# Optimization experiments

Hardware: AMD Instinct MI355X
Metric: run time of the kernel (lower is better)

## Reference

```python
import jax, jax.numpy as jnp
import numpy as np

N_NODES = 50000
N_EDGES = 1600000
HID = 64
CUT_D = 4.0   # cutoff_distance
CUT_ON = 3.8  # cutoff_onset


def setup_inputs() -> dict:
    key = jax.random.key(0)
    ks = jax.random.split(key, 12)
    x = jax.random.normal(ks[0], (N_NODES, HID), jnp.float32)
    x0 = jax.random.normal(ks[1], (N_NODES, HID), jnp.float32)
    y = jax.random.normal(ks[2], (N_EDGES, HID), jnp.float32)
    # bond lengths in [0, 5) to exercise the smooth cutoff region around 3.8-4.0
    bondlength = jax.random.uniform(ks[3], (N_EDGES,), jnp.float32) * 5.0
    src = jax.random.randint(ks[4], (N_EDGES,), 0, N_NODES, jnp.int32)
    dst = jax.random.randint(ks[5], (N_EDGES,), 0, N_NODES, jnp.int32)
    s = 1.0 / np.sqrt(HID)
    Wsg = jax.random.normal(ks[6], (HID, 1), jnp.float32) * s
    Wdg = jax.random.normal(ks[7], (HID, 1), jnp.float32) * s
    Weg = jax.random.normal(ks[8], (HID, 1), jnp.float32) * s
    Wsp = jax.random.normal(ks[9], (HID, 4), jnp.float32) * s
    Wdp = jax.random.normal(ks[10], (HID, 4), jnp.float32) * s
    bsg = jnp.zeros((1,), jnp.float32)
    bdg = jnp.zeros((1,), jnp.float32)
    beg = jnp.zeros((1,), jnp.float32)
    bsp = jnp.zeros((4,), jnp.float32)  # = log([1,1,1,1])
    return dict(x=x, x0=x0, y=y, bondlength=bondlength, src=src, dst=dst,
                Wsg=Wsg, bsg=bsg, Wdg=Wdg, bdg=bdg, Weg=Weg, beg=beg,
                Wsp=Wsp, bsp=bsp, Wdp=Wdp)


def _cutoff(r):
    D = 0.5 * (CUT_D - CUT_ON)  # 0.1
    R = CUT_D - D               # 3.9
    c = jnp.where(r < R - D, jnp.ones_like(r),
                  0.5 - 0.5 * jnp.sin(jnp.pi * (r - R) / (2 * D)))
    return jnp.where(r > R + D, jnp.zeros_like(r), c)


def reference(x, x0, y, bondlength, src, dst,
              Wsg, bsg, Wdg, bdg, Weg, beg, Wsp, bsp, Wdp):
    # BondOrderConv: per-edge gated sigmoid (u_add_v of node gates + edge gate)
    e_src = x @ Wsg + bsg          # [N,1]
    e_dst = x @ Wdg + bdg          # [N,1]
    m = e_src[src] + e_dst[dst] + (y @ Weg + beg)  # [E,1]
    bond_order = jax.nn.sigmoid(m)[:, 0]           # [E]

    # BondOrderInteraction: pairwise params via u_add_v, then pair potential
    p_src = x0 @ Wsp + bsp         # [N,4]
    p_dst = x0 @ Wdp               # [N,4] (no bias)
    params = jnp.exp(p_src[src] + p_dst[dst])      # [E,4]
    f_repulse = params[:, 0] * jnp.exp(-params[:, 1] * bondlength)
    f_attract = params[:, 2] * jnp.exp(-params[:, 3] * bondlength)
    V_pair = _cutoff(bondlength) * (f_repulse - bond_order * f_attract)  # [E]

    # copy_e / sum: scatter-add edge energies onto destination nodes
    atomwise_energy = jax.ops.segment_sum(V_pair, dst, num_segments=N_NODES)
    # AvgPooling readout (energy_units == 'eV/atom', single graph)
    energy = jnp.mean(atomwise_energy)
    return energy, atomwise_energy
```

## Files before the change

kernel.cpp:

```cpp
#include <hip/hip_runtime.h>
#include <hip/hip_bf16.h>

#define HID 64

typedef float f32x4 __attribute__((ext_vector_type(4)));

__global__ __launch_bounds__(256) void nbo_node_kernel(
    const float* __restrict__ x, const float* __restrict__ x0,
    const float* __restrict__ Wsg, const float* __restrict__ bsg,
    const float* __restrict__ Wdg, const float* __restrict__ bdg,
    const float* __restrict__ Wsp, const float* __restrict__ bsp,
    const float* __restrict__ Wdp,
    float* __restrict__ esrc, float* __restrict__ edst,
    float4* __restrict__ ps4, float4* __restrict__ pd4, int N)
{
    __shared__ float4 s_wsg[16];
    __shared__ float4 s_wdg[16];
    __shared__ float4 s_wsp[64];
    __shared__ float4 s_wdp[64];

    const int tid = threadIdx.x;
    if (tid < 16) {
        s_wsg[tid] = ((const float4*)Wsg)[tid];
        s_wdg[tid] = ((const float4*)Wdg)[tid];
    }
    if (tid < 64) {
        s_wsp[tid] = ((const float4*)Wsp)[tid];
        s_wdp[tid] = ((const float4*)Wdp)[tid];
    }
    __syncthreads();

    const int n = blockIdx.x * 256 + tid;
    if (n >= N) return;

    const float4* xv  = (const float4*)(x  + (size_t)n * HID);
    const float4* x0v = (const float4*)(x0 + (size_t)n * HID);

    float  asg = 0.f, adg = 0.f;
    float4 asp = make_float4(0.f, 0.f, 0.f, 0.f);
    float4 adp = make_float4(0.f, 0.f, 0.f, 0.f);

#pragma unroll
    for (int j = 0; j < 16; ++j) {
        const float4 a = xv[j];
        const float4 b = x0v[j];
        const float4 g = s_wsg[j];
        const float4 h = s_wdg[j];
        asg += a.x * g.x + a.y * g.y + a.z * g.z + a.w * g.w;
        adg += a.x * h.x + a.y * h.y + a.z * h.z + a.w * h.w;
#pragma unroll
        for (int c = 0; c < 4; ++c) {
            const float bx = (&b.x)[c];
            const float4 sp = s_wsp[4 * j + c];
            const float4 dp = s_wdp[4 * j + c];
            asp.x += bx * sp.x; asp.y += bx * sp.y;
            asp.z += bx * sp.z; asp.w += bx * sp.w;
            adp.x += bx * dp.x; adp.y += bx * dp.y;
            adp.z += bx * dp.z; adp.w += bx * dp.w;
        }
    }

    esrc[n] = asg + bsg[0];
    edst[n] = adg + bdg[0];
    ps4[n] = make_float4(asp.x + bsp[0], asp.y + bsp[1],
                         asp.z + bsp[2], asp.w + bsp[3]);
    pd4[n] = adp;
}

__global__ __launch_bounds__(256) void nbo_edge_kernel(
    const float* __restrict__ y, const float* __restrict__ bl,
    const int* __restrict__ src, const int* __restrict__ dst,
    const float* __restrict__ Weg, const float* __restrict__ beg,
    const float* __restrict__ esrc, const float* __restrict__ edst,
    const float4* __restrict__ ps4, const float4* __restrict__ pd4,
    float* __restrict__ out, int E, float invN)
{
    __shared__ float4 s_weg[16];
    const int tid = threadIdx.x;
    if (tid < 16) s_weg[tid] = ((const float4*)Weg)[tid];
    __syncthreads();

    const int e = blockIdx.x * 256 + tid;
    float V = 0.f;
    if (e < E) {
        const float r = bl[e];
        if (r <= 4.0f) {
            const int s = src[e];
            const int d = dst[e];

            const f32x4* yv = (const f32x4*)(y + (size_t)e * HID);
            float dotv = 0.f;
#pragma unroll
            for (int j = 0; j < 16; ++j) {
                const f32x4 a = __builtin_nontemporal_load(yv + j);
                const float4 w = s_weg[j];
                dotv += a.x * w.x + a.y * w.y + a.z * w.z + a.w * w.w;
            }

            const float m  = esrc[s] + edst[d] + dotv + beg[0];
            const float bo = 1.0f / (1.0f + __expf(-m));

            const float4 p1 = ps4[s];
            const float4 p2 = pd4[d];
            const float P1 = __expf(p1.y + p2.y);
            const float P3 = __expf(p1.w + p2.w);
            const float f_rep = __expf(p1.x + p2.x - P1 * r);
            const float f_att = __expf(p1.z + p2.z - P3 * r);

            const float cut = (r < 3.8f)
                ? 1.0f
                : (0.5f - 0.5f * __sinf(15.707963267948966f * (r - 3.9f)));

            V = cut * (f_rep - bo * f_att);
            atomicAdd(out + 1 + d, V);
        }
    }

#pragma unroll
    for (int off = 32; off > 0; off >>= 1)
        V += __shfl_down(V, off);

    __shared__ float s_wsum[4];
    const int wid  = tid >> 6;
    const int lane = tid & 63;
    if (lane == 0) s_wsum[wid] = V;
    __syncthreads();
    if (tid == 0) {
        const float bsum = s_wsum[0] + s_wsum[1] + s_wsum[2] + s_wsum[3];
        atomicAdd(out, bsum * invN);
    }
}

extern "C" void kernel_launch(void* const* d_in, const int* in_sizes, int n_in,
                              void* d_out, int out_size, void* d_ws, size_t ws_size,
                              hipStream_t stream) {
    const float* x   = (const float*)d_in[0];
    const float* x0  = (const float*)d_in[1];
    const float* y   = (const float*)d_in[2];
    const float* bl  = (const float*)d_in[3];
    const int*   src = (const int*)d_in[4];
    const int*   dst = (const int*)d_in[5];
    const float* Wsg = (const float*)d_in[6];
    const float* bsg = (const float*)d_in[7];
    const float* Wdg = (const float*)d_in[8];
    const float* bdg = (const float*)d_in[9];
    const float* Weg = (const float*)d_in[10];
    const float* beg = (const float*)d_in[11];
    const float* Wsp = (const float*)d_in[12];
    const float* bsp = (const float*)d_in[13];
    const float* Wdp = (const float*)d_in[14];

    const int N = in_sizes[0] / HID;
    const int E = in_sizes[3];

    float* out = (float*)d_out;
    float* ws  = (float*)d_ws;

    float*  w_esrc = ws;
    float*  w_edst = ws + (size_t)N;
    float4* w_ps4  = (float4*)(ws + 2 * (size_t)N);
    float4* w_pd4  = (float4*)(ws + 2 * (size_t)N + 4 * (size_t)N);

    (void)hipMemsetAsync(d_out, 0, (size_t)out_size * sizeof(float), stream);

    nbo_node_kernel<<<(N + 255) / 256, 256, 0, stream>>>(
        x, x0, Wsg, bsg, Wdg, bdg, Wsp, bsp, Wdp,
        w_esrc, w_edst, w_ps4, w_pd4, N);

    nbo_edge_kernel<<<(E + 255) / 256, 256, 0, stream>>>(
        y, bl, src, dst, Weg, beg,
        w_esrc, w_edst, w_ps4, w_pd4,
        out, E, 1.0f / (float)N);
}
```

Measured before the change: 708.9 us.

## Pack per-node gate and pair params together and hoist edge feature loads

Packs each node's pair parameters and gate scalar into adjacent float4 records so gathers for src and dst hit one 32-byte region each instead of two separate arrays. Moves the src/dst index loads and the y dot product ahead of the cutoff branch so they can issue without waiting on the bondlength compare, and drops the nontemporal load hint. The cost is that y rows are now read for every edge, including those beyond the cutoff that were previously skipped, which increases total streamed bytes.

```diff
diff --git a/kernel.cpp b/kernel.cpp
--- a/kernel.cpp
+++ b/kernel.cpp
@@ -2,8 +2,6 @@
 #include <hip/hip_bf16.h>
 
 #define HID 64
-
-typedef float f32x4 __attribute__((ext_vector_type(4)));
 
 __global__ __launch_bounds__(256) void nbo_node_kernel(
     const float* __restrict__ x, const float* __restrict__ x0,
@@ -11,8 +9,7 @@
     const float* __restrict__ Wdg, const float* __restrict__ bdg,
     const float* __restrict__ Wsp, const float* __restrict__ bsp,
     const float* __restrict__ Wdp,
-    float* __restrict__ esrc, float* __restrict__ edst,
-    float4* __restrict__ ps4, float4* __restrict__ pd4, int N)
+    float4* __restrict__ spack, float4* __restrict__ dpack, int N)
 {
     __shared__ float4 s_wsg[16];
     __shared__ float4 s_wdg[16];
@@ -60,19 +57,18 @@
         }
     }
 
-    esrc[n] = asg + bsg[0];
-    edst[n] = adg + bdg[0];
-    ps4[n] = make_float4(asp.x + bsp[0], asp.y + bsp[1],
-                         asp.z + bsp[2], asp.w + bsp[3]);
-    pd4[n] = adp;
+    spack[2 * n]     = make_float4(asp.x + bsp[0], asp.y + bsp[1],
+                                   asp.z + bsp[2], asp.w + bsp[3]);
+    spack[2 * n + 1] = make_float4(asg + bsg[0], 0.f, 0.f, 0.f);
+    dpack[2 * n]     = adp;
+    dpack[2 * n + 1] = make_float4(adg + bdg[0], 0.f, 0.f, 0.f);
 }
 
 __global__ __launch_bounds__(256) void nbo_edge_kernel(
     const float* __restrict__ y, const float* __restrict__ bl,
     const int* __restrict__ src, const int* __restrict__ dst,
     const float* __restrict__ Weg, const float* __restrict__ beg,
-    const float* __restrict__ esrc, const float* __restrict__ edst,
-    const float4* __restrict__ ps4, const float4* __restrict__ pd4,
+    const float4* __restrict__ spack, const float4* __restrict__ dpack,
     float* __restrict__ out, int E, float invN)
 {
     __shared__ float4 s_weg[16];
@@ -84,24 +80,27 @@
     float V = 0.f;
     if (e < E) {
         const float r = bl[e];
+        const int   s = src[e];
+        const int   d = dst[e];
+
+        const float4* yv = (const float4*)(y + (size_t)e * HID);
+        float dotv = 0.f;
+#pragma unroll
+        for (int j = 0; j < 16; ++j) {
+            const float4 a = yv[j];
+            const float4 w = s_weg[j];
+            dotv += a.x * w.x + a.y * w.y + a.z * w.z + a.w * w.w;
+        }
+
         if (r <= 4.0f) {
-            const int s = src[e];
-            const int d = dst[e];
+            const float4 p1 = spack[2 * s];
+            const float  es = ((const float*)(spack + 2 * s + 1))[0];
+            const float4 p2 = dpack[2 * d];
+            const float  ed = ((const float*)(dpack + 2 * d + 1))[0];
 
-            const f32x4* yv = (const f32x4*)(y + (size_t)e * HID);
-            float dotv = 0.f;
-#pragma unroll
-            for (int j = 0; j < 16; ++j) {
-                const f32x4 a = __builtin_nontemporal_load(yv + j);
-                const float4 w = s_weg[j];
-                dotv += a.x * w.x + a.y * w.y + a.z * w.z + a.w * w.w;
-            }
-
-            const float m  = esrc[s] + edst[d] + dotv + beg[0];
+            const float m  = es + ed + dotv + beg[0];
             const float bo = 1.0f / (1.0f + __expf(-m));
 
-            const float4 p1 = ps4[s];
-            const float4 p2 = pd4[d];
             const float P1 = __expf(p1.y + p2.y);
             const float P3 = __expf(p1.w + p2.w);
             const float f_rep = __expf(p1.x + p2.x - P1 * r);
@@ -156,19 +155,17 @@
     float* out = (float*)d_out;
     float* ws  = (float*)d_ws;
 
-    float*  w_esrc = ws;
-    float*  w_edst = ws + (size_t)N;
-    float4* w_ps4  = (float4*)(ws + 2 * (size_t)N);
-    float4* w_pd4  = (float4*)(ws + 2 * (size_t)N + 4 * (size_t)N);
+    float4* w_spack = (float4*)ws;
+    float4* w_dpack = (float4*)ws + 2 * (size_t)N;
 
     (void)hipMemsetAsync(d_out, 0, (size_t)out_size * sizeof(float), stream);
 
     nbo_node_kernel<<<(N + 255) / 256, 256, 0, stream>>>(
         x, x0, Wsg, bsg, Wdg, bdg, Wsp, bsp, Wdp,
-        w_esrc, w_edst, w_ps4, w_pd4, N);
+        w_spack, w_dpack, N);
 
     nbo_edge_kernel<<<(E + 255) / 256, 256, 0, stream>>>(
         y, bl, src, dst, Weg, beg,
-        w_esrc, w_edst, w_ps4, w_pd4,
+        w_spack, w_dpack,
         out, E, 1.0f / (float)N);
 }
```

Result: faster. 617.3 us (-12.9%).
